# Kernel optimization log

Measured on AMD Instinct MI355X. Metric: run time of the kernel, lower is better.

Reference implementation:

```python
import jax, jax.numpy as jnp
import numpy as np

N, D, K, H, G = 200000, 256, 128, 4, 1024  # nodes, emb_dim, hidden, heads, graphs


def setup_inputs() -> dict:
    key = jax.random.key(0)
    k0, k1, k2, k3 = jax.random.split(key, 4)
    node_features = jax.random.normal(k0, (N, D), jnp.float32)
    segment_ids = jnp.sort(jax.random.randint(k1, (N,), 0, G)).astype(jnp.int32)
    W1 = jax.random.normal(k2, (H, D, K), jnp.float32) / np.float32(np.sqrt(D))
    b1 = jnp.zeros((H, K), jnp.float32)
    W2 = jax.random.normal(k3, (H, K), jnp.float32) / np.float32(np.sqrt(K))
    b2 = jnp.zeros((H,), jnp.float32)
    return {"node_features": node_features, "segment_ids": segment_ids,
            "num_graphs": G, "W1": W1, "b1": b1, "W2": W2, "b2": b2}


def _segment_softmax(scores, seg, num_segments):
    # scores: [N, H]; numerically-stable softmax within each graph segment, per head
    m = jax.ops.segment_max(scores, seg, num_segments=num_segments)  # [G, H]
    e = jnp.exp(scores - m[seg])
    s = jax.ops.segment_sum(e, seg, num_segments=num_segments)  # [G, H]
    return e / s[seg]


def reference(node_features, segment_ids, num_graphs, W1, b1, W2, b2):
    # Per-head MLP score for all heads at once: [N, H]
    h = jax.nn.relu(jnp.einsum('nd,hdk->nhk', node_features, W1) + b1)
    scores = jnp.einsum('nhk,hk->nh', h, W2) + b2
    # dgl.softmax_nodes per head == segment softmax over graph ids
    attn = _segment_softmax(scores, segment_ids, num_graphs)  # [N, H]
    # combine_type == 'mean': mean_h segment_sum(attn_h * x)
    # == segment_sum(mean_h(attn_h) * x) since the sum is linear in attn.
    avg_attn = attn.mean(axis=1)  # [N]
    weighted = avg_attn[:, None] * node_features  # [N, D]
    return jax.ops.segment_sum(weighted, segment_ids, num_segments=num_graphs)  # [G, D]
```

## Files before the change

kernel.cpp:

```cpp
#include <hip/hip_runtime.h>
#include <hip/hip_bf16.h>

typedef unsigned short u16;
typedef __attribute__((ext_vector_type(8))) __bf16 bf16x8;
typedef __attribute__((ext_vector_type(8))) u16 u16x8;
typedef __attribute__((ext_vector_type(4))) float f32x4;

__device__ __forceinline__ u16 f2bf(float f) {
    unsigned u = __float_as_uint(f);
    u += 0x7fffu + ((u >> 16) & 1u);
    return (u16)(u >> 16);
}

__device__ __forceinline__ void gl_lds16(const void* g, void* l) {
    __builtin_amdgcn_global_load_lds(
        (const __attribute__((address_space(1))) void*)g,
        (__attribute__((address_space(3))) void*)l, 16, 0, 0);
}

__global__ __launch_bounds__(256) void transpose_w1(const float* __restrict__ W1,
                                                    u16* __restrict__ W1T) {
    __shared__ u16 tile[64][132];
    const int t = threadIdx.x;
    const int h = blockIdx.x >> 2;
    const int dt = blockIdx.x & 3;
#pragma unroll
    for (int j = 0; j < 8; ++j) {
        int idx = j * 256 + t;
        int r = idx >> 5;
        int kq = idx & 31;
        float4 v = *reinterpret_cast<const float4*>(
            W1 + ((size_t)h * 256 + dt * 64 + r) * 128 + kq * 4);
        ushort4 o;
        o.x = f2bf(v.x); o.y = f2bf(v.y); o.z = f2bf(v.z); o.w = f2bf(v.w);
        *reinterpret_cast<ushort4*>(&tile[r][kq * 4]) = o;
    }
    __syncthreads();
#pragma unroll
    for (int j = 0; j < 4; ++j) {
        int idx = j * 256 + t;
        int k = idx >> 3;
        int c8 = idx & 7;
        u16x8 o;
#pragma unroll
        for (int e = 0; e < 8; ++e) o[e] = tile[c8 * 8 + e][k];
        *reinterpret_cast<u16x8*>(W1T + ((size_t)h * 128 + k) * 256 + dt * 64 + c8 * 8) = o;
    }
}

__global__ __launch_bounds__(512, 4) void score_kernel(
        const float* __restrict__ x, const u16* __restrict__ W1T,
        const float* __restrict__ b1, const float* __restrict__ W2,
        const float* __restrict__ b2, float* __restrict__ scores, int N) {
    __shared__ u16 xb[16384];
    __shared__ u16 sA[16384];
    __shared__ float pr[4][4][16];

    const int t = threadIdx.x;
    const int wave = t >> 6;
    const int lane = t & 63;
    const int l15 = lane & 15;
    const int quad = lane >> 4;
    const int hh = wave >> 1;
    const int half = wave & 1;
    const int n0 = blockIdx.x * 64;

    const u16* asrc = W1T + ((size_t)hh * 128 + half * 64 + l15) * 256 + quad * 8;
    auto stageA = [&](int ks) {
#pragma unroll
        for (int j = 0; j < 4; ++j)
            gl_lds16(asrc + j * 4096 + ks * 32, &sA[(size_t)(wave * 4 + j) * 512]);
    };
    stageA(0);

    {
        const int n = t >> 3;
        const int ks = t & 7;
        int nn = n0 + n; if (nn >= N) nn = N - 1;
        const float* src = x + (size_t)nn * 256 + ks * 32;
        float4 v[8];
#pragma unroll
        for (int i = 0; i < 8; ++i)
            v[i] = *reinterpret_cast<const float4*>(src + i * 4);
        const int nf = n >> 4;
        const int r15 = n & 15;
#pragma unroll
        for (int kcq = 0; kcq < 4; ++kcq) {
            const int q = (kcq * 16 + r15) ^ (kcq << 1);
            u16x8 o;
            float4 vA = v[2 * kcq], vB = v[2 * kcq + 1];
            o[0] = f2bf(vA.x); o[1] = f2bf(vA.y); o[2] = f2bf(vA.z); o[3] = f2bf(vA.w);
            o[4] = f2bf(vB.x); o[5] = f2bf(vB.y); o[6] = f2bf(vB.z); o[7] = f2bf(vB.w);
            *reinterpret_cast<u16x8*>(&xb[((ks * 4 + nf) * 64 + q) * 8]) = o;
        }
    }

    const int qr = lane ^ ((lane >> 4) << 1);
    const u16* xrd = xb + qr * 8;
    const u16* abase = &sA[(size_t)wave * 2048 + lane * 8];

    __syncthreads();

    f32x4 acc[4][4] = {};
    for (int ks = 0; ks < 8; ++ks) {
        bf16x8 a[4], b[4];
#pragma unroll
        for (int j = 0; j < 4; ++j)
            a[j] = *reinterpret_cast<const bf16x8*>(abase + j * 512);
#pragma unroll
        for (int nf = 0; nf < 4; ++nf)
            b[nf] = *reinterpret_cast<const bf16x8*>(xrd + (ks * 4 + nf) * 512);
        __syncthreads();
        if (ks < 7) stageA(ks + 1);
#pragma unroll
        for (int fr = 0; fr < 4; ++fr)
#pragma unroll
            for (int nf = 0; nf < 4; ++nf)
                acc[fr][nf] = __builtin_amdgcn_mfma_f32_16x16x32_bf16(
                    a[fr], b[nf], acc[fr][nf], 0, 0, 0);
        __syncthreads();
    }

    float4 b1v[4], w2v[4];
#pragma unroll
    for (int fr = 0; fr < 4; ++fr) {
        int rb = hh * 128 + half * 64 + fr * 16 + quad * 4;
        b1v[fr] = *reinterpret_cast<const float4*>(b1 + rb);
        w2v[fr] = *reinterpret_cast<const float4*>(W2 + rb);
    }
    float p[4];
#pragma unroll
    for (int nf = 0; nf < 4; ++nf) {
        float pp = 0.f;
#pragma unroll
        for (int fr = 0; fr < 4; ++fr) {
            f32x4 c = acc[fr][nf];
            pp += fmaxf(c[0] + b1v[fr].x, 0.f) * w2v[fr].x
                + fmaxf(c[1] + b1v[fr].y, 0.f) * w2v[fr].y
                + fmaxf(c[2] + b1v[fr].z, 0.f) * w2v[fr].z
                + fmaxf(c[3] + b1v[fr].w, 0.f) * w2v[fr].w;
        }
        pp += __shfl_xor(pp, 16, 64);
        pp += __shfl_xor(pp, 32, 64);
        p[nf] = pp;
    }
    if (half == 1 && lane < 16) {
#pragma unroll
        for (int nf = 0; nf < 4; ++nf) pr[hh][nf][lane] = p[nf];
    }
    __syncthreads();
    if (half == 0 && lane < 16) {
        const float b2v = b2[hh];
#pragma unroll
        for (int nf = 0; nf < 4; ++nf) {
            int n = n0 + nf * 16 + lane;
            if (n < N)
                scores[(size_t)n * 4 + hh] = p[nf] + pr[hh][nf][lane] + b2v;
        }
    }
}

__device__ __forceinline__ int lower_bound(const int* __restrict__ a, int n, int v) {
    int lo = 0, hi = n;
    while (lo < hi) {
        int mid = (lo + hi) >> 1;
        if (a[mid] < v) lo = mid + 1; else hi = mid;
    }
    return lo;
}

__global__ __launch_bounds__(256) void starts_kernel(
        const int* __restrict__ seg, int* __restrict__ starts, int N, int G) {
    int g = blockIdx.x * 256 + threadIdx.x;
    if (g > G) return;
    if (g == 0)      starts[0] = 0;
    else if (g == G) starts[G] = N;
    else             starts[g] = lower_bound(seg, N, g);
}

__global__ __launch_bounds__(512) void pool_kernel(
        const float* __restrict__ x, const float4* __restrict__ scores4,
        const int* __restrict__ starts, float* __restrict__ out) {
    __shared__ float4 red[8];
    __shared__ float wl[1024];
    __shared__ float partial[512];
    const int g = blockIdx.x;
    const int t = threadIdx.x;
    const int lane = t & 63;
    const int wv = t >> 6;
    const int start = starts[g];
    const int end = starts[g + 1];
    const int len = end - start;

    float* og = out + (size_t)g * 256;
    if (len == 0) { if (t < 256) og[t] = 0.f; return; }

    float4 mx = make_float4(-3.4e38f, -3.4e38f, -3.4e38f, -3.4e38f);
    for (int i = start + t; i < end; i += 512) {
        float4 s = scores4[i];
        mx.x = fmaxf(mx.x, s.x); mx.y = fmaxf(mx.y, s.y);
        mx.z = fmaxf(mx.z, s.z); mx.w = fmaxf(mx.w, s.w);
    }
#pragma unroll
    for (int off = 1; off < 64; off <<= 1) {
        mx.x = fmaxf(mx.x, __shfl_xor(mx.x, off, 64));
        mx.y = fmaxf(mx.y, __shfl_xor(mx.y, off, 64));
        mx.z = fmaxf(mx.z, __shfl_xor(mx.z, off, 64));
        mx.w = fmaxf(mx.w, __shfl_xor(mx.w, off, 64));
    }
    if (lane == 0) red[wv] = mx;
    __syncthreads();
#pragma unroll
    for (int w = 1; w < 8; ++w) {
        mx.x = fmaxf(red[0].x, red[w].x) > mx.x ? fmaxf(red[0].x, red[w].x) : mx.x;
    }
    {
        float4 r = red[0];
        mx = r;
#pragma unroll
        for (int w = 1; w < 8; ++w) {
            float4 q = red[w];
            mx.x = fmaxf(mx.x, q.x); mx.y = fmaxf(mx.y, q.y);
            mx.z = fmaxf(mx.z, q.z); mx.w = fmaxf(mx.w, q.w);
        }
    }
    __syncthreads();

    float4 sm = make_float4(0.f, 0.f, 0.f, 0.f);
    for (int i = start + t; i < end; i += 512) {
        float4 s = scores4[i];
        sm.x += expf(s.x - mx.x); sm.y += expf(s.y - mx.y);
        sm.z += expf(s.z - mx.z); sm.w += expf(s.w - mx.w);
    }
#pragma unroll
    for (int off = 1; off < 64; off <<= 1) {
        sm.x += __shfl_xor(sm.x, off, 64);
        sm.y += __shfl_xor(sm.y, off, 64);
        sm.z += __shfl_xor(sm.z, off, 64);
        sm.w += __shfl_xor(sm.w, off, 64);
    }
    if (lane == 0) red[wv] = sm;
    __syncthreads();
    float4 inv;
    {
        float4 s0 = red[0];
#pragma unroll
        for (int w = 1; w < 8; ++w) {
            float4 q = red[w];
            s0.x += q.x; s0.y += q.y; s0.z += q.z; s0.w += q.w;
        }
        inv.x = 1.f / s0.x; inv.y = 1.f / s0.y;
        inv.z = 1.f / s0.z; inv.w = 1.f / s0.w;
    }

    const int col = t & 255;
    const int hf = t >> 8;
    float acc = 0.f;
    for (int c = 0; c < len; c += 1024) {
        const int cl = min(1024, len - c);
        __syncthreads();
        for (int i = t; i < cl; i += 512) {
            float4 s = scores4[start + c + i];
            wl[i] = 0.25f * (expf(s.x - mx.x) * inv.x + expf(s.y - mx.y) * inv.y +
                             expf(s.z - mx.z) * inv.z + expf(s.w - mx.w) * inv.w);
        }
        __syncthreads();
        const float* xp = x + (size_t)(start + c) * 256 + col;
        int jb = hf * 8;
        for (; jb + 8 <= cl; jb += 16) {
            float xv[8];
#pragma unroll
            for (int jj = 0; jj < 8; ++jj) xv[jj] = xp[(size_t)(jb + jj) * 256];
#pragma unroll
            for (int jj = 0; jj < 8; ++jj) acc += wl[jb + jj] * xv[jj];
        }
        if (jb < cl) {
            const int je = min(jb + 8, cl);
            for (int j = jb; j < je; ++j) acc += wl[j] * xp[(size_t)j * 256];
        }
    }
    partial[t] = acc;
    __syncthreads();
    if (t < 256) og[t] = partial[t] + partial[t + 256];
}

extern "C" void kernel_launch(void* const* d_in, const int* in_sizes, int n_in,
                              void* d_out, int out_size, void* d_ws, size_t ws_size,
                              hipStream_t stream) {
    const float* x  = (const float*)d_in[0];
    const int* seg  = (const int*)d_in[1];
    const float* W1 = (const float*)d_in[3];
    const float* b1 = (const float*)d_in[4];
    const float* W2 = (const float*)d_in[5];
    const float* b2 = (const float*)d_in[6];
    float* out = (float*)d_out;

    const int N = in_sizes[0] / 256;
    const int G = 1024;

    char* ws = (char*)d_ws;
    float* scores = (float*)ws;
    u16* W1T      = (u16*)(ws + (size_t)N * 16);
    int* starts   = (int*)(ws + (size_t)N * 16 + 262144);

    transpose_w1<<<16, 256, 0, stream>>>(W1, W1T);
    starts_kernel<<<(G + 256) / 256, 256, 0, stream>>>(seg, starts, N, G);
    score_kernel<<<(N + 63) / 64, 512, 0, stream>>>(x, W1T, b1, W2, b2, scores, N);
    pool_kernel<<<G, 512, 0, stream>>>(x, (const float4*)scores, starts, out);
}
```

Measured before the change: 421.6 us.

## Split score kernel per head with register-resident W1 and double-buffered x tiles

Restructures the score kernel so each block handles one head over 512 nodes, keeping that head's W1 slice in registers instead of restaging it through LDS every k-step. The x tiles are double-buffered in LDS, and the next tile's global load overlaps with the current MFMA work, removing per-k-step barriers. In exchange, x is read once per head (four times in total), relying on L2/cache locality between adjacent blocks. A dead redundant max loop in the pool kernel is also removed.

```diff
diff --git a/kernel.cpp b/kernel.cpp
--- a/kernel.cpp
+++ b/kernel.cpp
@@ -10,12 +10,6 @@
     unsigned u = __float_as_uint(f);
     u += 0x7fffu + ((u >> 16) & 1u);
     return (u16)(u >> 16);
-}
-
-__device__ __forceinline__ void gl_lds16(const void* g, void* l) {
-    __builtin_amdgcn_global_load_lds(
-        (const __attribute__((address_space(1))) void*)g,
-        (__attribute__((address_space(3))) void*)l, 16, 0, 0);
 }
 
 __global__ __launch_bounds__(256) void transpose_w1(const float* __restrict__ W1,
@@ -48,114 +42,121 @@
     }
 }
 
-__global__ __launch_bounds__(512, 4) void score_kernel(
+__global__ __launch_bounds__(256, 2) void score_kernel(
         const float* __restrict__ x, const u16* __restrict__ W1T,
         const float* __restrict__ b1, const float* __restrict__ W2,
         const float* __restrict__ b2, float* __restrict__ scores, int N) {
-    __shared__ u16 xb[16384];
-    __shared__ u16 sA[16384];
-    __shared__ float pr[4][4][16];
+    __shared__ u16 xb[2][16384];
+    __shared__ float pr[2][4][4][16];
 
     const int t = threadIdx.x;
     const int wave = t >> 6;
     const int lane = t & 63;
     const int l15 = lane & 15;
     const int quad = lane >> 4;
-    const int hh = wave >> 1;
-    const int half = wave & 1;
-    const int n0 = blockIdx.x * 64;
-
-    const u16* asrc = W1T + ((size_t)hh * 128 + half * 64 + l15) * 256 + quad * 8;
-    auto stageA = [&](int ks) {
-#pragma unroll
-        for (int j = 0; j < 4; ++j)
-            gl_lds16(asrc + j * 4096 + ks * 32, &sA[(size_t)(wave * 4 + j) * 512]);
-    };
-    stageA(0);
-
+    const int h = blockIdx.x & 3;
+    const int c0 = (blockIdx.x >> 2) * 512;
+
+    bf16x8 a[2][8];
     {
-        const int n = t >> 3;
-        const int ks = t & 7;
-        int nn = n0 + n; if (nn >= N) nn = N - 1;
-        const float* src = x + (size_t)nn * 256 + ks * 32;
-        float4 v[8];
-#pragma unroll
-        for (int i = 0; i < 8; ++i)
-            v[i] = *reinterpret_cast<const float4*>(src + i * 4);
-        const int nf = n >> 4;
-        const int r15 = n & 15;
-#pragma unroll
-        for (int kcq = 0; kcq < 4; ++kcq) {
-            const int q = (kcq * 16 + r15) ^ (kcq << 1);
-            u16x8 o;
-            float4 vA = v[2 * kcq], vB = v[2 * kcq + 1];
-            o[0] = f2bf(vA.x); o[1] = f2bf(vA.y); o[2] = f2bf(vA.z); o[3] = f2bf(vA.w);
-            o[4] = f2bf(vB.x); o[5] = f2bf(vB.y); o[6] = f2bf(vB.z); o[7] = f2bf(vB.w);
-            *reinterpret_cast<u16x8*>(&xb[((ks * 4 + nf) * 64 + q) * 8]) = o;
-        }
-    }
-
-    const int qr = lane ^ ((lane >> 4) << 1);
-    const u16* xrd = xb + qr * 8;
-    const u16* abase = &sA[(size_t)wave * 2048 + lane * 8];
-
-    __syncthreads();
-
-    f32x4 acc[4][4] = {};
-    for (int ks = 0; ks < 8; ++ks) {
-        bf16x8 a[4], b[4];
-#pragma unroll
-        for (int j = 0; j < 4; ++j)
-            a[j] = *reinterpret_cast<const bf16x8*>(abase + j * 512);
-#pragma unroll
-        for (int nf = 0; nf < 4; ++nf)
-            b[nf] = *reinterpret_cast<const bf16x8*>(xrd + (ks * 4 + nf) * 512);
-        __syncthreads();
-        if (ks < 7) stageA(ks + 1);
-#pragma unroll
-        for (int fr = 0; fr < 4; ++fr)
-#pragma unroll
-            for (int nf = 0; nf < 4; ++nf)
-                acc[fr][nf] = __builtin_amdgcn_mfma_f32_16x16x32_bf16(
-                    a[fr], b[nf], acc[fr][nf], 0, 0, 0);
-        __syncthreads();
-    }
-
-    float4 b1v[4], w2v[4];
-#pragma unroll
-    for (int fr = 0; fr < 4; ++fr) {
-        int rb = hh * 128 + half * 64 + fr * 16 + quad * 4;
+        const u16* ab = W1T + ((size_t)h * 128 + wave * 32 + l15) * 256 + quad * 8;
+#pragma unroll
+        for (int fr = 0; fr < 2; ++fr)
+#pragma unroll
+            for (int ks = 0; ks < 8; ++ks)
+                a[fr][ks] = *reinterpret_cast<const bf16x8*>(ab + fr * 4096 + ks * 32);
+    }
+    float4 b1v[2], w2v[2];
+#pragma unroll
+    for (int fr = 0; fr < 2; ++fr) {
+        int rb = h * 128 + wave * 32 + fr * 16 + quad * 4;
         b1v[fr] = *reinterpret_cast<const float4*>(b1 + rb);
         w2v[fr] = *reinterpret_cast<const float4*>(W2 + rb);
     }
-    float p[4];
-#pragma unroll
-    for (int nf = 0; nf < 4; ++nf) {
-        float pp = 0.f;
-#pragma unroll
-        for (int fr = 0; fr < 4; ++fr) {
-            f32x4 c = acc[fr][nf];
-            pp += fmaxf(c[0] + b1v[fr].x, 0.f) * w2v[fr].x
-                + fmaxf(c[1] + b1v[fr].y, 0.f) * w2v[fr].y
-                + fmaxf(c[2] + b1v[fr].z, 0.f) * w2v[fr].z
-                + fmaxf(c[3] + b1v[fr].w, 0.f) * w2v[fr].w;
-        }
-        pp += __shfl_xor(pp, 16, 64);
-        pp += __shfl_xor(pp, 32, 64);
-        p[nf] = pp;
-    }
-    if (half == 1 && lane < 16) {
-#pragma unroll
-        for (int nf = 0; nf < 4; ++nf) pr[hh][nf][lane] = p[nf];
-    }
-    __syncthreads();
-    if (half == 0 && lane < 16) {
-        const float b2v = b2[hh];
+    const float b2v = b2[h];
+
+    const int nrow = wave * 16 + (lane >> 2);
+    const int koff = (lane & 3) * 8;
+    const int l_t = ((lane & 3) << 4) | (lane >> 2);
+    const int qw = l_t ^ ((l_t >> 4) << 1);
+    auto loadX = [&](int n0, float4* v) {
+        int nn = n0 + nrow; if (nn >= N) nn = N - 1;
+        const float* src = x + (size_t)nn * 256 + koff;
+#pragma unroll
+        for (int i = 0; i < 8; ++i) {
+            v[2 * i]     = *reinterpret_cast<const float4*>(src + i * 32);
+            v[2 * i + 1] = *reinterpret_cast<const float4*>(src + i * 32 + 4);
+        }
+    };
+    auto writeX = [&](int buf, const float4* v) {
+        u16* dst = &xb[buf][wave * 512 + qw * 8];
+#pragma unroll
+        for (int i = 0; i < 8; ++i) {
+            u16x8 o;
+            o[0] = f2bf(v[2*i].x);   o[1] = f2bf(v[2*i].y);
+            o[2] = f2bf(v[2*i].z);   o[3] = f2bf(v[2*i].w);
+            o[4] = f2bf(v[2*i+1].x); o[5] = f2bf(v[2*i+1].y);
+            o[6] = f2bf(v[2*i+1].z); o[7] = f2bf(v[2*i+1].w);
+            *reinterpret_cast<u16x8*>(dst + i * 2048) = o;
+        }
+    };
+
+    const int qr = lane ^ ((lane >> 4) << 1);
+    const int nt = min(8, (N - c0 + 63) >> 6);
+
+    float4 v[16];
+    loadX(c0, v);
+    writeX(0, v);
+    __syncthreads();
+
+    for (int tt = 0; tt < nt; ++tt) {
+        const int cur = tt & 1;
+        const int n0 = c0 + tt * 64;
+        if (tt + 1 < nt) loadX(n0 + 64, v);
+
+        f32x4 acc[2][4] = {};
+        const u16* xrd = &xb[cur][qr * 8];
+#pragma unroll
+        for (int ks = 0; ks < 8; ++ks) {
+            bf16x8 b[4];
+#pragma unroll
+            for (int nf = 0; nf < 4; ++nf)
+                b[nf] = *reinterpret_cast<const bf16x8*>(xrd + (ks * 4 + nf) * 512);
+#pragma unroll
+            for (int fr = 0; fr < 2; ++fr)
+#pragma unroll
+                for (int nf = 0; nf < 4; ++nf)
+                    acc[fr][nf] = __builtin_amdgcn_mfma_f32_16x16x32_bf16(
+                        a[fr][ks], b[nf], acc[fr][nf], 0, 0, 0);
+        }
+
+        float p[4];
 #pragma unroll
         for (int nf = 0; nf < 4; ++nf) {
-            int n = n0 + nf * 16 + lane;
-            if (n < N)
-                scores[(size_t)n * 4 + hh] = p[nf] + pr[hh][nf][lane] + b2v;
+            float pp = 0.f;
+#pragma unroll
+            for (int fr = 0; fr < 2; ++fr) {
+                f32x4 c = acc[fr][nf];
+                pp += fmaxf(c[0] + b1v[fr].x, 0.f) * w2v[fr].x
+                    + fmaxf(c[1] + b1v[fr].y, 0.f) * w2v[fr].y
+                    + fmaxf(c[2] + b1v[fr].z, 0.f) * w2v[fr].z
+                    + fmaxf(c[3] + b1v[fr].w, 0.f) * w2v[fr].w;
+            }
+            pp += __shfl_xor(pp, 16, 64);
+            pp += __shfl_xor(pp, 32, 64);
+            p[nf] = pp;
+        }
+        if (lane < 16) {
+#pragma unroll
+            for (int nf = 0; nf < 4; ++nf) pr[cur][wave][nf][l15] = p[nf];
+        }
+        if (tt + 1 < nt) writeX(cur ^ 1, v);
+        __syncthreads();
+        if (lane < 16) {
+            float s = pr[cur][0][wave][l15] + pr[cur][1][wave][l15]
+                    + pr[cur][2][wave][l15] + pr[cur][3][wave][l15];
+            int n = n0 + wave * 16 + l15;
+            if (n < N) scores[(size_t)n * 4 + h] = s + b2v;
         }
     }
 }
@@ -210,10 +211,6 @@
     }
     if (lane == 0) red[wv] = mx;
     __syncthreads();
-#pragma unroll
-    for (int w = 1; w < 8; ++w) {
-        mx.x = fmaxf(red[0].x, red[w].x) > mx.x ? fmaxf(red[0].x, red[w].x) : mx.x;
-    }
     {
         float4 r = red[0];
         mx = r;
@@ -303,8 +300,9 @@
     u16* W1T      = (u16*)(ws + (size_t)N * 16);
     int* starts   = (int*)(ws + (size_t)N * 16 + 262144);
 
+    const int chunks = (N + 511) / 512;
     transpose_w1<<<16, 256, 0, stream>>>(W1, W1T);
     starts_kernel<<<(G + 256) / 256, 256, 0, stream>>>(seg, starts, N, G);
-    score_kernel<<<(N + 63) / 64, 512, 0, stream>>>(x, W1T, b1, W2, b2, scores, N);
+    score_kernel<<<chunks * 4, 256, 0, stream>>>(x, W1T, b1, W2, b2, scores, N);
     pool_kernel<<<G, 512, 0, stream>>>(x, (const float4*)scores, starts, out);
 }
```

After: 393.5 us. 6.7% less time.
